# Optimization experiments

Measured on AMD Instinct MI355X. Metric: run time of the kernel, lower is better.

The kernel has to match this reference:

```python
import jax, jax.numpy as jnp
import numpy as np

K = 16
N = 32
NUM_WORDS = 2 ** K  # 65536


def build_codebook(G):
    """Faithful translation of MinDistanceDecoder.init_codebook.

    Returns (possible_words [2^k, k], possible_codewords [2^k, n],
             possible_codewords_llrs [2^k, n]) in float32.
    """
    Gf = G.astype(jnp.float32)
    # coefs = round(2 ** linspace(1, k, k)) = [2, 4, ..., 2^k]
    coefs = jnp.round(2.0 ** jnp.linspace(1.0, float(K), K))  # [k]
    # linspace(0, 2^k-1, 2^k) hits exact integers; floor is identity here
    idx = jnp.floor(jnp.linspace(0.0, float(NUM_WORDS) - 1.0, NUM_WORDS))  # [2^k]
    pw = idx[:, None] % coefs[None, :]  # [2^k, k]
    sub = jnp.concatenate([jnp.zeros((NUM_WORDS, 1), jnp.float32), pw[:, :-1]], axis=-1)
    possible_words = (pw - sub) / (coefs / 2.0)  # binary bits, LSB-first
    possible_codewords = (possible_words @ Gf) % 2.0  # [2^k, n]
    possible_codewords_llrs = -1.0 * (possible_codewords * 2.0 - 1.0)  # +/-1 BPSK LLR signs
    return possible_words, possible_codewords, possible_codewords_llrs


def setup_inputs() -> dict:
    key = jax.random.key(0)
    k1, k2 = jax.random.split(key)
    noisy_symbols = jax.random.normal(k1, (64, N), dtype=jnp.float32)
    G = jax.random.randint(k2, (K, N), 0, 2, dtype=jnp.int32)
    sigma2 = jnp.ones((1,), dtype=jnp.float32)
    return {"noisy_symbols": noisy_symbols, "G": G, "sigma2": sigma2}


def reference(noisy_symbols, G, sigma2):
    possible_words, possible_codewords, cw_llrs = build_codebook(G)
    llrs = -4.0 * noisy_symbols.astype(jnp.float32) / sigma2  # [B, n]
    max_abs = jnp.max(jnp.abs(llrs))  # global max over broadcast tensor == max over llrs
    # mean |llr - max_abs * codeword_llr| per (batch, codeword): [B, 2^k]
    dist = jnp.mean(jnp.abs(llrs[:, None, :] - max_abs * cw_llrs[None, :, :]), axis=-1)
    best = jnp.argmin(dist, axis=-1)  # [B]
    # return_words=True -> gather message words
    return possible_words[best]  # [B, k]
```

## Files before the change

### kernel.cpp

```cpp
#include <hip/hip_runtime.h>
#include <stdint.h>

#define B 64
#define N 32
#define K 16
#define NUM_WORDS 65536
#define BLOCKS 512
#define WPB 128
#define LLR_PAD 65

typedef unsigned long long u64;

__global__ __launch_bounds__(256) void mdd_corr(
    const float* __restrict__ noisy,
    const int* __restrict__ G,
    const float* __restrict__ sigma2,
    u64* __restrict__ ws_keys)
{
    __shared__ uint32_t g_rows[K];
    __shared__ __align__(16) uint32_t cw_lds[WPB];
    __shared__ float T_lds[8 * 16 * 64];
    __shared__ float llr_t[N * LLR_PAD];
    __shared__ float bestf_lds[4 * 64];
    __shared__ uint32_t bestw_lds[4 * 64];

    const int tid = threadIdx.x;
    const int l = tid & 63;
    const int wv = tid >> 6;

    if (tid < K) {
        uint32_t r = 0;
        #pragma unroll
        for (int n = 0; n < N; ++n)
            r |= (uint32_t)(G[tid * N + n] & 1) << n;
        g_rows[tid] = r;
    }

    const float scale = -4.0f / sigma2[0];
    for (int i = tid; i < B * N; i += 256) {
        int n = i & 31, bb = i >> 5;
        llr_t[n * LLR_PAD + bb] = scale * noisy[i];
    }
    __syncthreads();

    if (tid < WPB) {
        uint32_t w = blockIdx.x * WPB + tid;
        uint32_t cw = 0;
        #pragma unroll
        for (int k = 0; k < K; ++k)
            cw ^= g_rows[k] & (0u - ((w >> k) & 1u));
        cw_lds[tid] = cw;
    }

    for (int j = wv; j < 8; j += 4) {
        float l0 = llr_t[(4 * j + 0) * LLR_PAD + l];
        float l1 = llr_t[(4 * j + 1) * LLR_PAD + l];
        float l2 = llr_t[(4 * j + 2) * LLR_PAD + l];
        float l3 = llr_t[(4 * j + 3) * LLR_PAD + l];
        float A[4] = { l0 + l1, -l0 + l1, l0 - l1, -l0 - l1 };
        float C[4] = { l2 + l3, -l2 + l3, l2 - l3, -l2 - l3 };
        float* Tj = &T_lds[j * 1024 + l];
        #pragma unroll
        for (int v = 0; v < 16; ++v)
            Tj[v * 64] = A[v & 3] + C[v >> 2];
    }
    __syncthreads();

    const uint4* cw4 = reinterpret_cast<const uint4*>(cw_lds);
    const float* Tl = &T_lds[l];
    float bestf = -INFINITY;
    uint32_t bestw = 0;
    const uint32_t wbase = blockIdx.x * WPB + wv * 32;

    #pragma unroll
    for (int wq = 0; wq < 8; ++wq) {
        uint4 c4 = cw4[wv * 8 + wq];
        #pragma unroll
        for (int e = 0; e < 4; ++e) {
            uint32_t cw = (e == 0) ? c4.x : (e == 1) ? c4.y : (e == 2) ? c4.z : c4.w;
            float r0 = Tl[0 * 1024 + ((cw >> 0) & 15u) * 64];
            float r1 = Tl[1 * 1024 + ((cw >> 4) & 15u) * 64];
            float r2 = Tl[2 * 1024 + ((cw >> 8) & 15u) * 64];
            float r3 = Tl[3 * 1024 + ((cw >> 12) & 15u) * 64];
            float r4 = Tl[4 * 1024 + ((cw >> 16) & 15u) * 64];
            float r5 = Tl[5 * 1024 + ((cw >> 20) & 15u) * 64];
            float r6 = Tl[6 * 1024 + ((cw >> 24) & 15u) * 64];
            float r7 = Tl[7 * 1024 + ((cw >> 28) & 15u) * 64];
            float c = ((r0 + r1) + (r2 + r3)) + ((r4 + r5) + (r6 + r7));
            uint32_t w = wbase + wq * 4 + e;
            bool g = c > bestf;
            bestw = g ? w : bestw;
            bestf = g ? c : bestf;
        }
    }

    bestf_lds[wv * 64 + l] = bestf;
    bestw_lds[wv * 64 + l] = bestw;
    __syncthreads();

    if (tid < B) {
        float f = bestf_lds[tid];
        uint32_t w = bestw_lds[tid];
        #pragma unroll
        for (int v = 1; v < 4; ++v) {
            float f2 = bestf_lds[v * 64 + tid];
            uint32_t w2 = bestw_lds[v * 64 + tid];
            bool g = f2 > f;
            w = g ? w2 : w;
            f = g ? f2 : f;
        }
        uint32_t bits = __float_as_uint(f);
        uint32_t mono = (bits & 0x80000000u) ? ~bits : (bits | 0x80000000u);
        u64 key = ((u64)mono << 16) | (u64)(0xFFFFu - w);
        ws_keys[tid * BLOCKS + blockIdx.x] = key;
    }
}

__global__ __launch_bounds__(64) void mdd_reduce(
    const u64* __restrict__ ws_keys,
    float* __restrict__ out)
{
    const int b = blockIdx.x;
    const int lane = threadIdx.x;
    const ulonglong2* p = reinterpret_cast<const ulonglong2*>(ws_keys + (size_t)b * BLOCKS);

    u64 m = 0;
    #pragma unroll
    for (int i = 0; i < 4; ++i) {
        ulonglong2 v = p[i * 64 + lane];
        u64 a = v.x > v.y ? v.x : v.y;
        m = a > m ? a : m;
    }
    #pragma unroll
    for (int off = 32; off > 0; off >>= 1) {
        u64 o = __shfl_xor(m, off, 64);
        m = o > m ? o : m;
    }
    uint32_t w = 0xFFFFu - (uint32_t)(m & 0xFFFFu);
    if (lane < K) out[b * K + lane] = (float)((w >> lane) & 1u);
}

extern "C" void kernel_launch(void* const* d_in, const int* in_sizes, int n_in,
                              void* d_out, int out_size, void* d_ws, size_t ws_size,
                              hipStream_t stream) {
    const float* noisy = (const float*)d_in[0];
    const int* G = (const int*)d_in[1];
    const float* sigma2 = (const float*)d_in[2];
    float* out = (float*)d_out;
    u64* ws_keys = (u64*)d_ws;

    (void)in_sizes; (void)n_in; (void)out_size; (void)ws_size;

    mdd_corr<<<BLOCKS, 256, 0, stream>>>(noisy, G, sigma2, ws_keys);
    mdd_reduce<<<B, 64, 0, stream>>>(ws_keys, out);
}
```

Before: 13.80 us.

## Replace upper LDS tables with register sign-flip sums and atomic-max reduction

Shrinks the 4-bit lookup tables from 8 to 5. The last 12 codeword bits are now handled by flipping the sign bits of per-lane LLRs held in registers and summing them, which cuts LDS gathers per codeword. The per-block partial writes followed by a separate reduce kernel are replaced by a 64-bit atomicMax into zeroed slots, with a small output kernel. G is also loaded as int4. This trades extra ALU work and an added memset launch for fewer LDS reads and a simpler reduction.

```diff
diff --git a/kernel.cpp b/kernel.cpp
--- a/kernel.cpp
+++ b/kernel.cpp
@@ -8,6 +8,9 @@
 #define BLOCKS 512
 #define WPB 128
 #define LLR_PAD 65
+#define NTAB 5
+#define NV 12
+#define SLOT_STRIDE 8
 
 typedef unsigned long long u64;
 
@@ -15,11 +18,11 @@
     const float* __restrict__ noisy,
     const int* __restrict__ G,
     const float* __restrict__ sigma2,
-    u64* __restrict__ ws_keys)
+    u64* __restrict__ slots)
 {
     __shared__ uint32_t g_rows[K];
     __shared__ __align__(16) uint32_t cw_lds[WPB];
-    __shared__ float T_lds[8 * 16 * 64];
+    __shared__ float T_lds[NTAB * 16 * 64];
     __shared__ float llr_t[N * LLR_PAD];
     __shared__ float bestf_lds[4 * 64];
     __shared__ uint32_t bestw_lds[4 * 64];
@@ -29,10 +32,16 @@
     const int wv = tid >> 6;
 
     if (tid < K) {
+        const int4* G4 = reinterpret_cast<const int4*>(G) + tid * 8;
         uint32_t r = 0;
         #pragma unroll
-        for (int n = 0; n < N; ++n)
-            r |= (uint32_t)(G[tid * N + n] & 1) << n;
+        for (int m = 0; m < 8; ++m) {
+            int4 gv = G4[m];
+            r |= (uint32_t)(gv.x & 1) << (4 * m + 0);
+            r |= (uint32_t)(gv.y & 1) << (4 * m + 1);
+            r |= (uint32_t)(gv.z & 1) << (4 * m + 2);
+            r |= (uint32_t)(gv.w & 1) << (4 * m + 3);
+        }
         g_rows[tid] = r;
     }
 
@@ -52,7 +61,7 @@
         cw_lds[tid] = cw;
     }
 
-    for (int j = wv; j < 8; j += 4) {
+    for (int j = wv; j < NTAB; j += 4) {
         float l0 = llr_t[(4 * j + 0) * LLR_PAD + l];
         float l1 = llr_t[(4 * j + 1) * LLR_PAD + l];
         float l2 = llr_t[(4 * j + 2) * LLR_PAD + l];
@@ -64,6 +73,11 @@
         for (int v = 0; v < 16; ++v)
             Tj[v * 64] = A[v & 3] + C[v >> 2];
     }
+
+    uint32_t lau[NV];
+    #pragma unroll
+    for (int v = 0; v < NV; ++v)
+        lau[v] = __float_as_uint(llr_t[(4 * NTAB + v) * LLR_PAD + l]);
     __syncthreads();
 
     const uint4* cw4 = reinterpret_cast<const uint4*>(cw_lds);
@@ -83,10 +97,11 @@
             float r2 = Tl[2 * 1024 + ((cw >> 8) & 15u) * 64];
             float r3 = Tl[3 * 1024 + ((cw >> 12) & 15u) * 64];
             float r4 = Tl[4 * 1024 + ((cw >> 16) & 15u) * 64];
-            float r5 = Tl[5 * 1024 + ((cw >> 20) & 15u) * 64];
-            float r6 = Tl[6 * 1024 + ((cw >> 24) & 15u) * 64];
-            float r7 = Tl[7 * 1024 + ((cw >> 28) & 15u) * 64];
-            float c = ((r0 + r1) + (r2 + r3)) + ((r4 + r5) + (r6 + r7));
+            float vs = 0.0f;
+            #pragma unroll
+            for (int v = 0; v < NV; ++v)
+                vs += __uint_as_float(lau[v] ^ ((cw << (11 - v)) & 0x80000000u));
+            float c = ((r0 + r1) + (r2 + r3)) + (r4 + vs);
             uint32_t w = wbase + wq * 4 + e;
             bool g = c > bestf;
             bestw = g ? w : bestw;
@@ -112,32 +127,25 @@
         uint32_t bits = __float_as_uint(f);
         uint32_t mono = (bits & 0x80000000u) ? ~bits : (bits | 0x80000000u);
         u64 key = ((u64)mono << 16) | (u64)(0xFFFFu - w);
-        ws_keys[tid * BLOCKS + blockIdx.x] = key;
+        atomicMax(&slots[tid * SLOT_STRIDE], key);
     }
 }
 
-__global__ __launch_bounds__(64) void mdd_reduce(
-    const u64* __restrict__ ws_keys,
+__global__ __launch_bounds__(256) void mdd_out(
+    const u64* __restrict__ slots,
     float* __restrict__ out)
 {
-    const int b = blockIdx.x;
-    const int lane = threadIdx.x;
-    const ulonglong2* p = reinterpret_cast<const ulonglong2*>(ws_keys + (size_t)b * BLOCKS);
-
-    u64 m = 0;
-    #pragma unroll
-    for (int i = 0; i < 4; ++i) {
-        ulonglong2 v = p[i * 64 + lane];
-        u64 a = v.x > v.y ? v.x : v.y;
-        m = a > m ? a : m;
+    __shared__ uint32_t w_lds[B];
+    const int tid = threadIdx.x;
+    if (tid < B) {
+        u64 f = slots[tid * SLOT_STRIDE];
+        w_lds[tid] = 0xFFFFu - (uint32_t)(f & 0xFFFFull);
     }
-    #pragma unroll
-    for (int off = 32; off > 0; off >>= 1) {
-        u64 o = __shfl_xor(m, off, 64);
-        m = o > m ? o : m;
+    __syncthreads();
+    for (int i = tid; i < B * K; i += 256) {
+        int b2 = i >> 4, kk = i & 15;
+        out[i] = (float)((w_lds[b2] >> kk) & 1u);
     }
-    uint32_t w = 0xFFFFu - (uint32_t)(m & 0xFFFFu);
-    if (lane < K) out[b * K + lane] = (float)((w >> lane) & 1u);
 }
 
 extern "C" void kernel_launch(void* const* d_in, const int* in_sizes, int n_in,
@@ -147,10 +155,11 @@
     const int* G = (const int*)d_in[1];
     const float* sigma2 = (const float*)d_in[2];
     float* out = (float*)d_out;
-    u64* ws_keys = (u64*)d_ws;
+    u64* slots = (u64*)d_ws;
 
     (void)in_sizes; (void)n_in; (void)out_size; (void)ws_size;
 
-    mdd_corr<<<BLOCKS, 256, 0, stream>>>(noisy, G, sigma2, ws_keys);
-    mdd_reduce<<<B, 64, 0, stream>>>(ws_keys, out);
+    hipMemsetAsync(slots, 0, B * SLOT_STRIDE * sizeof(u64), stream);
+    mdd_corr<<<BLOCKS, 256, 0, stream>>>(noisy, G, sigma2, slots);
+    mdd_out<<<1, 256, 0, stream>>>(slots, out);
 }
```

New measurement: 26.76 us. +93.9%, slower.

## Use 7-bit lookup tables plus sign-flip tail bits for codeword correlation

Applied to the files above, without the earlier changes.

Replaces the eight 4-bit partial-sum tables with four 7-bit tables (128 entries each) covering 28 bits. The remaining 4 bits are handled by XORing sign bits into the register-held LLRs, which cuts LDS loads per codeword from 8 to 4. Blocks go from 512x256 threads to 256x512 threads with 256 words each, and the G packing uses vectorized int4 loads. The cost is a much larger table (128 KB of LDS, which limits occupancy) and a longer table-build phase per block.

```diff
diff --git a/kernel.cpp b/kernel.cpp
--- a/kernel.cpp
+++ b/kernel.cpp
@@ -5,39 +5,48 @@
 #define N 32
 #define K 16
 #define NUM_WORDS 65536
-#define BLOCKS 512
-#define WPB 128
+#define NBLK 256
+#define WPB 256
+#define NTHR 512
 #define LLR_PAD 65
 
 typedef unsigned long long u64;
 
-__global__ __launch_bounds__(256) void mdd_corr(
+static __device__ __forceinline__ u64 umax64(u64 a, u64 b) { return a > b ? a : b; }
+
+__global__ __launch_bounds__(NTHR) void mdd_corr(
     const float* __restrict__ noisy,
     const int* __restrict__ G,
     const float* __restrict__ sigma2,
-    u64* __restrict__ ws_keys)
+    u64* __restrict__ ws)
 {
     __shared__ uint32_t g_rows[K];
     __shared__ __align__(16) uint32_t cw_lds[WPB];
-    __shared__ float T_lds[8 * 16 * 64];
+    __shared__ float T_lds[4 * 128 * 64];
     __shared__ float llr_t[N * LLR_PAD];
-    __shared__ float bestf_lds[4 * 64];
-    __shared__ uint32_t bestw_lds[4 * 64];
+    __shared__ float bestf_lds[8 * 64];
+    __shared__ uint32_t bestw_lds[8 * 64];
 
     const int tid = threadIdx.x;
     const int l = tid & 63;
     const int wv = tid >> 6;
 
     if (tid < K) {
+        const int4* G4 = reinterpret_cast<const int4*>(G) + tid * 8;
         uint32_t r = 0;
         #pragma unroll
-        for (int n = 0; n < N; ++n)
-            r |= (uint32_t)(G[tid * N + n] & 1) << n;
+        for (int m = 0; m < 8; ++m) {
+            int4 gv = G4[m];
+            r |= (uint32_t)(gv.x & 1) << (4 * m + 0);
+            r |= (uint32_t)(gv.y & 1) << (4 * m + 1);
+            r |= (uint32_t)(gv.z & 1) << (4 * m + 2);
+            r |= (uint32_t)(gv.w & 1) << (4 * m + 3);
+        }
         g_rows[tid] = r;
     }
 
     const float scale = -4.0f / sigma2[0];
-    for (int i = tid; i < B * N; i += 256) {
+    for (int i = tid; i < B * N; i += NTHR) {
         int n = i & 31, bb = i >> 5;
         llr_t[n * LLR_PAD + bb] = scale * noisy[i];
     }
@@ -52,18 +61,40 @@
         cw_lds[tid] = cw;
     }
 
-    for (int j = wv; j < 8; j += 4) {
-        float l0 = llr_t[(4 * j + 0) * LLR_PAD + l];
-        float l1 = llr_t[(4 * j + 1) * LLR_PAD + l];
-        float l2 = llr_t[(4 * j + 2) * LLR_PAD + l];
-        float l3 = llr_t[(4 * j + 3) * LLR_PAD + l];
-        float A[4] = { l0 + l1, -l0 + l1, l0 - l1, -l0 - l1 };
-        float C[4] = { l2 + l3, -l2 + l3, l2 - l3, -l2 - l3 };
-        float* Tj = &T_lds[j * 1024 + l];
+    {
+        const int g = wv & 3, h = wv >> 2;
+        float l0 = llr_t[(7 * g + 0) * LLR_PAD + l];
+        float l1 = llr_t[(7 * g + 1) * LLR_PAD + l];
+        float l2 = llr_t[(7 * g + 2) * LLR_PAD + l];
+        float l3 = llr_t[(7 * g + 3) * LLR_PAD + l];
+        float l4 = llr_t[(7 * g + 4) * LLR_PAD + l];
+        float l5 = llr_t[(7 * g + 5) * LLR_PAD + l];
+        float l6 = llr_t[(7 * g + 6) * LLR_PAD + l];
+        float l6s = h ? -l6 : l6;
+        float P[4] = { l0 + l1, -l0 + l1, l0 - l1, -l0 - l1 };
+        float A[8];
         #pragma unroll
-        for (int v = 0; v < 16; ++v)
-            Tj[v * 64] = A[v & 3] + C[v >> 2];
+        for (int a = 0; a < 8; ++a)
+            A[a] = (a & 4) ? (P[a & 3] - l2) : (P[a & 3] + l2);
+        float Q[4] = { l3 + l4, -l3 + l4, l3 - l4, -l3 - l4 };
+        float R[8];
+        #pragma unroll
+        for (int r = 0; r < 8; ++r)
+            R[r] = (r & 4) ? (Q[r & 3] - l5) : (Q[r & 3] + l5);
+        float Cp[8];
+        #pragma unroll
+        for (int c = 0; c < 8; ++c)
+            Cp[c] = R[c] + l6s;
+        float* Tg = &T_lds[g * 8192 + h * 64 * 64 + l];
+        #pragma unroll
+        for (int j = 0; j < 64; ++j)
+            Tg[j * 64] = A[j & 7] + Cp[j >> 3];
     }
+
+    uint32_t lau0 = __float_as_uint(llr_t[28 * LLR_PAD + l]);
+    uint32_t lau1 = __float_as_uint(llr_t[29 * LLR_PAD + l]);
+    uint32_t lau2 = __float_as_uint(llr_t[30 * LLR_PAD + l]);
+    uint32_t lau3 = __float_as_uint(llr_t[31 * LLR_PAD + l]);
     __syncthreads();
 
     const uint4* cw4 = reinterpret_cast<const uint4*>(cw_lds);
@@ -78,15 +109,15 @@
         #pragma unroll
         for (int e = 0; e < 4; ++e) {
             uint32_t cw = (e == 0) ? c4.x : (e == 1) ? c4.y : (e == 2) ? c4.z : c4.w;
-            float r0 = Tl[0 * 1024 + ((cw >> 0) & 15u) * 64];
-            float r1 = Tl[1 * 1024 + ((cw >> 4) & 15u) * 64];
-            float r2 = Tl[2 * 1024 + ((cw >> 8) & 15u) * 64];
-            float r3 = Tl[3 * 1024 + ((cw >> 12) & 15u) * 64];
-            float r4 = Tl[4 * 1024 + ((cw >> 16) & 15u) * 64];
-            float r5 = Tl[5 * 1024 + ((cw >> 20) & 15u) * 64];
-            float r6 = Tl[6 * 1024 + ((cw >> 24) & 15u) * 64];
-            float r7 = Tl[7 * 1024 + ((cw >> 28) & 15u) * 64];
-            float c = ((r0 + r1) + (r2 + r3)) + ((r4 + r5) + (r6 + r7));
+            float r0 = Tl[0 * 8192 + ((cw >> 0) & 127u) * 64];
+            float r1 = Tl[1 * 8192 + ((cw >> 7) & 127u) * 64];
+            float r2 = Tl[2 * 8192 + ((cw >> 14) & 127u) * 64];
+            float r3 = Tl[3 * 8192 + ((cw >> 21) & 127u) * 64];
+            float v0 = __uint_as_float(lau0 ^ ((cw << 3) & 0x80000000u));
+            float v1 = __uint_as_float(lau1 ^ ((cw << 2) & 0x80000000u));
+            float v2 = __uint_as_float(lau2 ^ ((cw << 1) & 0x80000000u));
+            float v3 = __uint_as_float(lau3 ^ ((cw << 0) & 0x80000000u));
+            float c = ((r0 + r1) + (r2 + r3)) + ((v0 + v1) + (v2 + v3));
             uint32_t w = wbase + wq * 4 + e;
             bool g = c > bestf;
             bestw = g ? w : bestw;
@@ -102,7 +133,7 @@
         float f = bestf_lds[tid];
         uint32_t w = bestw_lds[tid];
         #pragma unroll
-        for (int v = 1; v < 4; ++v) {
+        for (int v = 1; v < 8; ++v) {
             float f2 = bestf_lds[v * 64 + tid];
             uint32_t w2 = bestw_lds[v * 64 + tid];
             bool g = f2 > f;
@@ -112,32 +143,26 @@
         uint32_t bits = __float_as_uint(f);
         uint32_t mono = (bits & 0x80000000u) ? ~bits : (bits | 0x80000000u);
         u64 key = ((u64)mono << 16) | (u64)(0xFFFFu - w);
-        ws_keys[tid * BLOCKS + blockIdx.x] = key;
+        ws[(size_t)tid * NBLK + blockIdx.x] = key;
     }
 }
 
-__global__ __launch_bounds__(64) void mdd_reduce(
-    const u64* __restrict__ ws_keys,
+__global__ __launch_bounds__(64) void mdd_out(
+    const u64* __restrict__ ws,
     float* __restrict__ out)
 {
     const int b = blockIdx.x;
-    const int lane = threadIdx.x;
-    const ulonglong2* p = reinterpret_cast<const ulonglong2*>(ws_keys + (size_t)b * BLOCKS);
+    const int t = threadIdx.x;
+    const u64* p = ws + (size_t)b * NBLK;
 
-    u64 m = 0;
-    #pragma unroll
-    for (int i = 0; i < 4; ++i) {
-        ulonglong2 v = p[i * 64 + lane];
-        u64 a = v.x > v.y ? v.x : v.y;
-        m = a > m ? a : m;
-    }
+    u64 m = umax64(umax64(p[t], p[t + 64]), umax64(p[t + 128], p[t + 192]));
     #pragma unroll
     for (int off = 32; off > 0; off >>= 1) {
         u64 o = __shfl_xor(m, off, 64);
-        m = o > m ? o : m;
+        m = umax64(m, o);
     }
-    uint32_t w = 0xFFFFu - (uint32_t)(m & 0xFFFFu);
-    if (lane < K) out[b * K + lane] = (float)((w >> lane) & 1u);
+    uint32_t w = 0xFFFFu - (uint32_t)(m & 0xFFFFull);
+    if (t < K) out[b * K + t] = (float)((w >> t) & 1u);
 }
 
 extern "C" void kernel_launch(void* const* d_in, const int* in_sizes, int n_in,
@@ -147,10 +172,10 @@
     const int* G = (const int*)d_in[1];
     const float* sigma2 = (const float*)d_in[2];
     float* out = (float*)d_out;
-    u64* ws_keys = (u64*)d_ws;
+    u64* ws = (u64*)d_ws;
 
     (void)in_sizes; (void)n_in; (void)out_size; (void)ws_size;
 
-    mdd_corr<<<BLOCKS, 256, 0, stream>>>(noisy, G, sigma2, ws_keys);
-    mdd_reduce<<<B, 64, 0, stream>>>(ws_keys, out);
+    mdd_corr<<<NBLK, NTHR, 0, stream>>>(noisy, G, sigma2, ws);
+    mdd_out<<<B, 64, 0, stream>>>(ws, out);
 }
```

Result: faster. 13.45 us (median of 2 runs) (-2.5%).
